# Performance work log

Hardware: AMD Instinct MI355X
Metric: run time of the kernel (lower is better)

Reference implementation:

```python
import jax, jax.numpy as jnp
import numpy as np

SMU_ALPHA = 0.25
SMU_MU = 1.0e6  # repo's act.SMU default: large mu -> smooth leaky-relu (max(x, alpha*x))

def smu(x):
    a = SMU_ALPHA
    return 0.5 * ((1.0 + a) * x + (1.0 - a) * x * jax.lax.erf(SMU_MU * (1.0 - a) * x))

def setup_inputs() -> dict:
    key = jax.random.key(0)
    ks = jax.random.split(key, 6)
    B, N, D = 8, 4096, 1024
    xavier = float(np.sqrt(6.0 / (D + D)))
    def lin_w(k):
        return jax.random.uniform(k, (D, D), jnp.float32, -xavier, xavier)
    return {
        "x": jax.random.normal(ks[0], (B, N, D), jnp.float32),
        "Wvr": lin_w(ks[1]), "bvr": jnp.zeros((D,), jnp.float32),
        "Wvi": lin_w(ks[2]), "bvi": jnp.zeros((D,), jnp.float32),
        "Wk": lin_w(ks[3]), "bk": jnp.zeros((D,), jnp.float32),
        "Wq": lin_w(ks[4]), "bq": jnp.zeros((D,), jnp.float32),
    }

def reference(x, Wvr, bvr, Wvi, bvi, Wk, bk, Wq, bq):
    # real input: real and imag branches both see x
    value_real = jnp.einsum('bnd,ed->bne', x, Wvr) + bvr
    value_imag = jnp.einsum('bnd,ed->bne', x, Wvi) + bvi
    # GLU: v_real * tanh(softplus(v_imag)); dropout disabled (p=0)
    value = value_real * jnp.tanh(jax.nn.softplus(value_imag))
    key_ = jnp.einsum('bnd,ed->bne', x, Wk) + bk
    query = jnp.einsum('bnd,ed->bne', x, Wq) + bq
    # L2 normalize along the sequence dim (dim=1)
    key_n = key_ / (jnp.linalg.norm(key_, axis=1, keepdims=True) + 1e-5)
    query_n = query / (jnp.linalg.norm(query, axis=1, keepdims=True) + 1e-5)
    feature_attn = smu(jnp.einsum('bnd,bne->bde', key_n, query_n))  # [B, D, D]
    return jnp.einsum('bnd,bde->bne', value, feature_attn)
```

## Files before the change

### kernel.cpp

```cpp
#include <hip/hip_runtime.h>
#include <math.h>

typedef __bf16 bf16x8 __attribute__((ext_vector_type(8)));
typedef float f32x4 __attribute__((ext_vector_type(4)));

#define MTOT 32768
#define DD   1024
#define NSEQ 4096
#define BB   8

__device__ __forceinline__ void async16(const void* gp, void* lp) {
  __builtin_amdgcn_global_load_lds(
      (__attribute__((address_space(1))) void*)(const_cast<void*>(gp)),
      (__attribute__((address_space(3))) void*)(lp), 16, 0, 0);
}

__device__ __forceinline__ unsigned short f2bf(float f) {
  union { float f; unsigned int u; } v; v.f = f;
  unsigned int r = v.u + 0x7fffu + ((v.u >> 16) & 1u);
  return (unsigned short)(r >> 16);
}
__device__ __forceinline__ float bf2f(unsigned short u) {
  union { unsigned int u; float f; } v; v.u = ((unsigned int)u) << 16; return v.f;
}

__device__ __forceinline__ unsigned lds_off(void* p) {
  return (unsigned)(unsigned long long)
      (__attribute__((address_space(3))) void*)p;
}
#define DSRI(dst, base, off) \
  asm volatile("ds_read_b128 %0, %1 offset:" #off : "=v"(dst) : "v"(base))

#define MFMA_ __builtin_amdgcn_mfma_f32_16x16x32_bf16

__global__ void cvt_bf16(const float* __restrict__ in, unsigned short* __restrict__ out, int n) {
  int i = (blockIdx.x * blockDim.x + threadIdx.x) * 8;
  if (i >= n) return;
  float4 a = *(const float4*)(in + i);
  float4 b = *(const float4*)(in + i + 4);
  ushort4 o0, o1;
  o0.x = f2bf(a.x); o0.y = f2bf(a.y); o0.z = f2bf(a.z); o0.w = f2bf(a.w);
  o1.x = f2bf(b.x); o1.y = f2bf(b.y); o1.z = f2bf(b.z); o1.w = f2bf(b.w);
  *(ushort4*)(out + i) = o0;
  *(ushort4*)(out + i + 4) = o1;
}

__global__ void cvt_w(const float* __restrict__ w0, const float* __restrict__ w1,
                      const float* __restrict__ w2, const float* __restrict__ w3,
                      unsigned short* __restrict__ out) {
  int z = blockIdx.y;
  const float* in = (z == 0) ? w0 : (z == 1) ? w1 : (z == 2) ? w2 : w3;
  int i = (blockIdx.x * blockDim.x + threadIdx.x) * 8;
  float4 a = *(const float4*)(in + i);
  float4 b = *(const float4*)(in + i + 4);
  ushort4 o0, o1;
  o0.x = f2bf(a.x); o0.y = f2bf(a.y); o0.z = f2bf(a.z); o0.w = f2bf(a.w);
  o1.x = f2bf(b.x); o1.y = f2bf(b.y); o1.z = f2bf(b.z); o1.w = f2bf(b.w);
  unsigned short* o = out + (size_t)z * DD * DD;
  *(ushort4*)(o + i) = o0;
  *(ushort4*)(o + i + 4) = o1;
}

template<int LDG>
__device__ __forceinline__ void stage32(const unsigned short* __restrict__ g,
                                        int row0, int k0,
                                        unsigned short* lds, int tid) {
#pragma unroll
  for (int l = 0; l < 2; ++l) {
    int u = l * 512 + tid;
    int r = u >> 2;
    int c = u & 3;
    async16(g + (size_t)(row0 + r) * LDG + k0 + c * 8, (char*)lds + u * 16);
  }
}

template<int LDG>
__device__ __forceinline__ void stage_half(const unsigned short* __restrict__ g,
                                           int row0, int k0,
                                           unsigned short* lds, int tid) {
#pragma unroll
  for (int l = 0; l < 2; ++l) {
    int u = l * 512 + tid;
    int r = u >> 3;
    int sl = (u & 7) ^ (r & 7);
    async16(g + (size_t)(row0 + r) * LDG + k0 + sl * 8, (char*)lds + u * 16);
  }
}

__global__ __launch_bounds__(512, 2) void proj_all(
    const unsigned short* __restrict__ xb,
    const unsigned short* __restrict__ Wb,
    const float* __restrict__ bvr, const float* __restrict__ bvi,
    const float* __restrict__ bk,  const float* __restrict__ bq,
    unsigned short* __restrict__ oVr, unsigned short* __restrict__ oVi,
    unsigned short* __restrict__ Kt,  unsigned short* __restrict__ Qt,
    float* __restrict__ rnacc) {
  __shared__ __align__(16) unsigned short smem[49152];

  const int bx = blockIdx.x;
  const int swz = (bx & 7) * 64 + (bx >> 3);
  const int m0 = (swz >> 2) * 256;
  const int n0 = (swz & 3) * 256;
  const int z = blockIdx.z;
  const unsigned short* W = Wb + (size_t)z * DD * DD;
  const float* bias = (z == 0) ? bvr : (z == 1) ? bvi : (z == 2) ? bk : bq;

  const int tid = threadIdx.x;
  const int w = tid >> 6, lane = tid & 63;
  const int wr = w >> 2, wc = w & 3;
  const int lq = lane >> 4, lr = lane & 15;
  const int arow0 = wr * 128 + lr;
  const int brow0 = wc * 64 + lr;

  f32x4 acc[8][4];
#pragma unroll
  for (int i = 0; i < 8; i++)
#pragma unroll
    for (int j = 0; j < 4; j++) acc[i][j] = (f32x4)(0.f);

  const int NT = 32;

  const unsigned sbase = lds_off(smem);
  unsigned aA[3], aB[3];
#pragma unroll
  for (int i = 0; i < 3; ++i) {
    aA[i] = sbase + i * 32768u + (unsigned)(arow0 * 64 + lq * 16);
    aB[i] = sbase + i * 32768u + 32768u / 2u + (unsigned)(brow0 * 64 + lq * 16);
  }

  bf16x8 A1[4], B0[2][4], A2[2][4];

  stage32<1024>(xb, m0, 0,  smem,                tid);
  stage32<1024>(W,  n0, 0,  smem + 8192,         tid);
  stage32<1024>(xb, m0, 32, smem + 16384,        tid);
  stage32<1024>(W,  n0, 32, smem + 16384 + 8192, tid);
  asm volatile("s_waitcnt vmcnt(4)" ::: "memory");
  __builtin_amdgcn_s_barrier();

  DSRI(A1[0],    aA[0], 0);    DSRI(A1[1],    aA[0], 1024);
  DSRI(A1[2],    aA[0], 2048); DSRI(A1[3],    aA[0], 3072);
  DSRI(B0[0][0], aB[0], 0);    DSRI(B0[0][1], aB[0], 1024);
  DSRI(B0[0][2], aB[0], 2048); DSRI(B0[0][3], aB[0], 3072);
  DSRI(A2[0][0], aA[0], 4096); DSRI(A2[0][1], aA[0], 5120);
  DSRI(A2[0][2], aA[0], 6144); DSRI(A2[0][3], aA[0], 7168);
  asm volatile("s_waitcnt lgkmcnt(4)" ::: "memory");
  __builtin_amdgcn_sched_barrier(0);
  __builtin_amdgcn_s_setprio(1);
#pragma unroll
  for (int mi = 0; mi < 4; ++mi)
#pragma unroll
    for (int nj = 0; nj < 4; ++nj)
      acc[mi][nj] = MFMA_(A1[mi], B0[0][nj], acc[mi][nj], 0, 0, 0);
  __builtin_amdgcn_s_setprio(0);
  __builtin_amdgcn_sched_barrier(0);
  asm volatile("s_waitcnt vmcnt(0)" ::: "memory");
  __builtin_amdgcn_s_barrier();

#pragma unroll
  for (int k = 0; k < NT - 1; ++k) {
    const int cs = k & 1, ns = (k + 1) & 1;
    const unsigned rA = aA[(k + 1) % 3], rB = aB[(k + 1) % 3];
    DSRI(A1[0],     rA, 0);    DSRI(A1[1],     rA, 1024);
    DSRI(A1[2],     rA, 2048); DSRI(A1[3],     rA, 3072);
    DSRI(B0[ns][0], rB, 0);    DSRI(B0[ns][1], rB, 1024);
    DSRI(B0[ns][2], rB, 2048); DSRI(B0[ns][3], rB, 3072);
    DSRI(A2[ns][0], rA, 4096); DSRI(A2[ns][1], rA, 5120);
    DSRI(A2[ns][2], rA, 6144); DSRI(A2[ns][3], rA, 7168);
    if (k + 2 < NT) {
      unsigned short* d = smem + ((k + 2) % 3) * 16384;
      stage32<1024>(xb, m0, (k + 2) * 32, d,        tid);
      stage32<1024>(W,  n0, (k + 2) * 32, d + 8192, tid);
    }
    asm volatile("s_waitcnt lgkmcnt(12)" ::: "memory");
    __builtin_amdgcn_sched_barrier(0);
    __builtin_amdgcn_s_setprio(1);
#pragma unroll
    for (int mi = 0; mi < 4; ++mi)
#pragma unroll
      for (int nj = 0; nj < 4; ++nj)
        acc[4 + mi][nj] = MFMA_(A2[cs][mi], B0[cs][nj], acc[4 + mi][nj], 0, 0, 0);
    __builtin_amdgcn_s_setprio(0);
    __builtin_amdgcn_sched_barrier(0);
    asm volatile("s_waitcnt lgkmcnt(4)" ::: "memory");
    __builtin_amdgcn_sched_barrier(0);
    __builtin_amdgcn_s_setprio(1);
#pragma unroll
    for (int mi = 0; mi < 4; ++mi)
#pragma unroll
      for (int nj = 0; nj < 4; ++nj)
        acc[mi][nj] = MFMA_(A1[mi], B0[ns][nj], acc[mi][nj], 0, 0, 0);
    __builtin_amdgcn_s_setprio(0);
    __builtin_amdgcn_sched_barrier(0);
    asm volatile("s_waitcnt vmcnt(0)" ::: "memory");
    __builtin_amdgcn_s_barrier();
  }
  asm volatile("s_waitcnt lgkmcnt(0)" ::: "memory");
  __builtin_amdgcn_sched_barrier(0);
#pragma unroll
  for (int mi = 0; mi < 4; ++mi)
#pragma unroll
    for (int nj = 0; nj < 4; ++nj)
      acc[4 + mi][nj] = MFMA_(A2[1][mi], B0[1][nj], acc[4 + mi][nj], 0, 0, 0);

  if (z < 2) {
    unsigned short* out = (z == 0) ? oVr : oVi;
#pragma unroll
    for (int nj = 0; nj < 4; ++nj) {
      int col = n0 + wc * 64 + nj * 16 + lr;
      float bv = bias[col];
#pragma unroll
      for (int mrep = 0; mrep < 8; ++mrep) {
        int rowb = m0 + wr * 128 + mrep * 16 + lq * 4;
#pragma unroll
        for (int r = 0; r < 4; ++r)
          out[(size_t)(rowb + r) * DD + col] = f2bf(acc[mrep][nj][r] + bv);
      }
    }
  } else {
    __syncthreads();
    unsigned short* outp = (z == 2) ? Kt : Qt;
    const int which = z - 2;
    const int b = m0 >> 12;
    const int nbase = m0 & 4095;
    float* racc = rnacc + which * (BB * DD) + b * DD;
    unsigned short* T = smem;
    const int SP2 = 264;
#pragma unroll
    for (int ch = 0; ch < 2; ++ch) {
      if ((wc >> 1) == ch) {
#pragma unroll
        for (int nj = 0; nj < 4; ++nj) {
          int cloc = (wc & 1) * 64 + nj * 16 + lr;
          float bv = bias[n0 + ch * 128 + cloc];
#pragma unroll
          for (int mrep = 0; mrep < 8; ++mrep) {
            int rowb = wr * 128 + mrep * 16 + lq * 4;
            ushort4 pk;
            pk.x = f2bf(acc[mrep][nj][0] + bv); pk.y = f2bf(acc[mrep][nj][1] + bv);
            pk.z = f2bf(acc[mrep][nj][2] + bv); pk.w = f2bf(acc[mrep][nj][3] + bv);
            *(ushort4*)(T + cloc * SP2 + rowb) = pk;
          }
        }
      }
      __syncthreads();
#pragma unroll
      for (int p = 0; p < 8; ++p) {
        int dl = p * 16 + (tid >> 5);
        int nc = (tid & 31) * 8;
        ushort4 v0 = *(const ushort4*)(T + dl * SP2 + nc);
        ushort4 v1 = *(const ushort4*)(T + dl * SP2 + nc + 4);
        int d = n0 + ch * 128 + dl;
        *(ushort4*)(outp + (size_t)(b * DD + d) * NSEQ + nbase + nc)     = v0;
        *(ushort4*)(outp + (size_t)(b * DD + d) * NSEQ + nbase + nc + 4) = v1;
        float s = bf2f(v0.x)*bf2f(v0.x) + bf2f(v0.y)*bf2f(v0.y) + bf2f(v0.z)*bf2f(v0.z) + bf2f(v0.w)*bf2f(v0.w)
                + bf2f(v1.x)*bf2f(v1.x) + bf2f(v1.y)*bf2f(v1.y) + bf2f(v1.z)*bf2f(v1.z) + bf2f(v1.w)*bf2f(v1.w);
#pragma unroll
        for (int off = 1; off < 32; off <<= 1) s += __shfl_xor(s, off, 32);
        if ((tid & 31) == 0) atomicAdd(&racc[d], s);
      }
      __syncthreads();
    }
  }
}

__global__ void finalize_rn(float* __restrict__ rn) {
  int i = blockIdx.x * blockDim.x + threadIdx.x;
  rn[i] = 1.f / (sqrtf(rn[i]) + 1e-5f);
}

__global__ void glu(unsigned short* __restrict__ V, const unsigned short* __restrict__ Vi, int n) {
  int i = (blockIdx.x * blockDim.x + threadIdx.x) * 8;
  if (i >= n) return;
  ushort4 r0 = *(const ushort4*)(V + i);
  ushort4 r1 = *(const ushort4*)(V + i + 4);
  ushort4 i0 = *(const ushort4*)(Vi + i);
  ushort4 i1 = *(const ushort4*)(Vi + i + 4);
  unsigned short vr[8] = {r0.x, r0.y, r0.z, r0.w, r1.x, r1.y, r1.z, r1.w};
  unsigned short vi[8] = {i0.x, i0.y, i0.z, i0.w, i1.x, i1.y, i1.z, i1.w};
  unsigned short o[8];
#pragma unroll
  for (int k = 0; k < 8; k++) {
    float a = bf2f(vr[k]), b = bf2f(vi[k]);
    float g;
    if (b > 10.f) g = 1.f;
    else { float t = __expf(b); float u = t * (t + 2.f); g = u / (u + 2.f); }
    o[k] = f2bf(a * g);
  }
  *(ushort4*)(V + i)     = make_ushort4(o[0], o[1], o[2], o[3]);
  *(ushort4*)(V + i + 4) = make_ushort4(o[4], o[5], o[6], o[7]);
}

__global__ __launch_bounds__(512, 2) void attn_gemm(
    const unsigned short* __restrict__ Qt, const unsigned short* __restrict__ Kt,
    const float* __restrict__ rn, unsigned short* __restrict__ fat) {
  __shared__ __align__(16) unsigned short smem[57344];

  const int b = blockIdx.z;
  const int d0 = blockIdx.x * 128;
  const int e0 = blockIdx.y * 256;
  const unsigned short* A  = Qt + (size_t)b * DD * NSEQ;
  const unsigned short* Bm = Kt + (size_t)b * DD * NSEQ;
  unsigned short* out = fat + (size_t)b * DD * DD;

  const int tid = threadIdx.x;
  const int w = tid >> 6, lane = tid & 63;
  const int wr = w >> 1, wc = w & 1;
  const int lq = lane >> 4, lr = lane & 15;
  const int sx = lr & 7;
  const int arow0 = wr * 64 + lr;
  const int brow0 = wc * 64 + lr;

  f32x4 acc[4][4];
#pragma unroll
  for (int i = 0; i < 4; i++)
#pragma unroll
    for (int j = 0; j < 4; j++) acc[i][j] = (f32x4)(0.f);

  const int NT = 64;

  const unsigned sbase = lds_off(smem);
  const unsigned sw0 = (unsigned)((lq ^ sx) << 4);
  const unsigned sw1 = (unsigned)(((4 | lq) ^ sx) << 4);
  unsigned aA0 = sbase + arow0 * 128 + sw0;
  unsigned aA1 = sbase + arow0 * 128 + sw1;
  unsigned aB0 = sbase + 32768 + brow0 * 128 + sw0;
  unsigned aB1 = sbase + 32768 + brow0 * 128 + sw1;

  stage_half<NSEQ>(A,  e0,       0,  smem,                 tid);
  stage_half<NSEQ>(A,  e0 + 128, 0,  smem + 8192,          tid);
  stage_half<NSEQ>(Bm, d0,       0,  smem + 16384,         tid);
  stage_half<NSEQ>(Bm, d0,       64, smem + 32768 + 16384, tid);
  asm volatile("s_waitcnt vmcnt(2)" ::: "memory");
  __builtin_amdgcn_s_barrier();

  for (int t = 0; t < NT; ++t) {
    bf16x8 bfr[4][2], aL[2][2];
    DSRI(aL[0][0], aA0, 0);    DSRI(aL[0][1], aA1, 0);
    DSRI(bfr[0][0], aB0, 0);    DSRI(bfr[0][1], aB1, 0);
    DSRI(bfr[1][0], aB0, 2048); DSRI(bfr[1][1], aB1, 2048);
    DSRI(bfr[2][0], aB0, 4096); DSRI(bfr[2][1], aB1, 4096);
    DSRI(bfr[3][0], aB0, 6144); DSRI(bfr[3][1], aB1, 6144);
    DSRI(aL[1][0], aA0, 2048); DSRI(aL[1][1], aA1, 2048);
    if (t + 1 < NT) {
      stage_half<NSEQ>(A, e0,       (t + 1) * 64, smem + ((t + 1) & 1) * 32768, tid);
      stage_half<NSEQ>(A, e0 + 128, (t + 1) * 64, smem + ((t + 1) & 1) * 32768 + 8192, tid);
    }
    __builtin_amdgcn_s_barrier();
    asm volatile("s_waitcnt lgkmcnt(2)" ::: "memory");
    __builtin_amdgcn_sched_barrier(0);
    __builtin_amdgcn_s_setprio(1);
#pragma unroll
    for (int nj = 0; nj < 4; ++nj) {
      acc[0][nj] = MFMA_(aL[0][0], bfr[nj][0], acc[0][nj], 0, 0, 0);
      acc[0][nj] = MFMA_(aL[0][1], bfr[nj][1], acc[0][nj], 0, 0, 0);
    }
    asm volatile("s_waitcnt lgkmcnt(0)" ::: "memory");
    __builtin_amdgcn_sched_barrier(0);
#pragma unroll
    for (int nj = 0; nj < 4; ++nj) {
      acc[1][nj] = MFMA_(aL[1][0], bfr[nj][0], acc[1][nj], 0, 0, 0);
      acc[1][nj] = MFMA_(aL[1][1], bfr[nj][1], acc[1][nj], 0, 0, 0);
    }
    __builtin_amdgcn_s_setprio(0);
    __builtin_amdgcn_sched_barrier(0);
    __builtin_amdgcn_s_barrier();

    bf16x8 aH[2][2];
    DSRI(aH[0][0], aA0, 4096); DSRI(aH[0][1], aA1, 4096);
    DSRI(aH[1][0], aA0, 6144); DSRI(aH[1][1], aA1, 6144);
    if (t + 2 < NT) {
      stage_half<NSEQ>(Bm, d0, (t + 2) * 64, smem + (t & 1) * 32768 + 16384, tid);
    }
    __builtin_amdgcn_s_barrier();
    asm volatile("s_waitcnt lgkmcnt(2)" ::: "memory");
    __builtin_amdgcn_sched_barrier(0);
    __builtin_amdgcn_s_setprio(1);
#pragma unroll
    for (int nj = 0; nj < 4; ++nj) {
      acc[2][nj] = MFMA_(aH[0][0], bfr[nj][0], acc[2][nj], 0, 0, 0);
      acc[2][nj] = MFMA_(aH[0][1], bfr[nj][1], acc[2][nj], 0, 0, 0);
    }
    asm volatile("s_waitcnt lgkmcnt(0)" ::: "memory");
    __builtin_amdgcn_sched_barrier(0);
#pragma unroll
    for (int nj = 0; nj < 4; ++nj) {
      acc[3][nj] = MFMA_(aH[1][0], bfr[nj][0], acc[3][nj], 0, 0, 0);
      acc[3][nj] = MFMA_(aH[1][1], bfr[nj][1], acc[3][nj], 0, 0, 0);
    }
    __builtin_amdgcn_s_setprio(0);
    __builtin_amdgcn_sched_barrier(0);
    if (t < NT - 2)       asm volatile("s_waitcnt vmcnt(2)" ::: "memory");
    else if (t == NT - 2) asm volatile("s_waitcnt vmcnt(0)" ::: "memory");
    __builtin_amdgcn_s_barrier();

    aA0 ^= 65536u; aA1 ^= 65536u; aB0 ^= 65536u; aB1 ^= 65536u;
  }

#pragma unroll
  for (int nj = 0; nj < 4; ++nj) {
    int col = d0 + wc * 64 + nj * 16 + lr;
    float rk = rn[b * DD + col];
#pragma unroll
    for (int mi = 0; mi < 4; ++mi) {
      int rowb = e0 + wr * 64 + mi * 16 + lq * 4;
#pragma unroll
      for (int r = 0; r < 4; ++r) {
        float rq = rn[BB * DD + b * DD + rowb + r];
        float c = acc[mi][nj][r] * rq * rk;
        c = (c > 0.f) ? c : 0.25f * c;
        out[(size_t)(rowb + r) * DD + col] = f2bf(c);
      }
    }
  }
}

__global__ __launch_bounds__(512, 2) void out_gemm(
    const unsigned short* __restrict__ V, const unsigned short* __restrict__ fat,
    float* __restrict__ out) {
  __shared__ __align__(16) unsigned short smem[49152];

  const int bx = blockIdx.x;
  const int swz = (bx & 7) * 64 + (bx >> 3);
  const int m0 = (swz >> 2) * 256;
  const int e0 = (swz & 3) * 256;
  const int b = m0 >> 12;
  const unsigned short* Bm = fat + (size_t)b * DD * DD;

  const int tid = threadIdx.x;
  const int w = tid >> 6, lane = tid & 63;
  const int wr = w >> 2, wc = w & 3;
  const int lq = lane >> 4, lr = lane & 15;
  const int arow0 = wr * 128 + lr;
  const int brow0 = wc * 64 + lr;

  f32x4 acc[8][4];
#pragma unroll
  for (int i = 0; i < 8; i++)
#pragma unroll
    for (int j = 0; j < 4; j++) acc[i][j] = (f32x4)(0.f);

  const int NT = 32;

  const unsigned sbase = lds_off(smem);
  unsigned aA[3], aB[3];
#pragma unroll
  for (int i = 0; i < 3; ++i) {
    aA[i] = sbase + i * 32768u + (unsigned)(arow0 * 64 + lq * 16);
    aB[i] = sbase + i * 32768u + 16384u + (unsigned)(brow0 * 64 + lq * 16);
  }

  bf16x8 A1[4], B0[2][4], A2[2][4];

  stage32<1024>(V,  m0, 0,  smem,                tid);
  stage32<1024>(Bm, e0, 0,  smem + 8192,         tid);
  stage32<1024>(V,  m0, 32, smem + 16384,        tid);
  stage32<1024>(Bm, e0, 32, smem + 16384 + 8192, tid);
  asm volatile("s_waitcnt vmcnt(4)" ::: "memory");
  __builtin_amdgcn_s_barrier();

  DSRI(A1[0],    aA[0], 0);    DSRI(A1[1],    aA[0], 1024);
  DSRI(A1[2],    aA[0], 2048); DSRI(A1[3],    aA[0], 3072);
  DSRI(B0[0][0], aB[0], 0);    DSRI(B0[0][1], aB[0], 1024);
  DSRI(B0[0][2], aB[0], 2048); DSRI(B0[0][3], aB[0], 3072);
  DSRI(A2[0][0], aA[0], 4096); DSRI(A2[0][1], aA[0], 5120);
  DSRI(A2[0][2], aA[0], 6144); DSRI(A2[0][3], aA[0], 7168);
  asm volatile("s_waitcnt lgkmcnt(4)" ::: "memory");
  __builtin_amdgcn_sched_barrier(0);
  __builtin_amdgcn_s_setprio(1);
#pragma unroll
  for (int mi = 0; mi < 4; ++mi)
#pragma unroll
    for (int nj = 0; nj < 4; ++nj)
      acc[mi][nj] = MFMA_(A1[mi], B0[0][nj], acc[mi][nj], 0, 0, 0);
  __builtin_amdgcn_s_setprio(0);
  __builtin_amdgcn_sched_barrier(0);
  asm volatile("s_waitcnt vmcnt(0)" ::: "memory");
  __builtin_amdgcn_s_barrier();

#pragma unroll
  for (int k = 0; k < NT - 1; ++k) {
    const int cs = k & 1, ns = (k + 1) & 1;
    const unsigned rA = aA[(k + 1) % 3], rB = aB[(k + 1) % 3];
    DSRI(A1[0],     rA, 0);    DSRI(A1[1],     rA, 1024);
    DSRI(A1[2],     rA, 2048); DSRI(A1[3],     rA, 3072);
    DSRI(B0[ns][0], rB, 0);    DSRI(B0[ns][1], rB, 1024);
    DSRI(B0[ns][2], rB, 2048); DSRI(B0[ns][3], rB, 3072);
    DSRI(A2[ns][0], rA, 4096); DSRI(A2[ns][1], rA, 5120);
    DSRI(A2[ns][2], rA, 6144); DSRI(A2[ns][3], rA, 7168);
    if (k + 2 < NT) {
      unsigned short* d = smem + ((k + 2) % 3) * 16384;
      stage32<1024>(V,  m0, (k + 2) * 32, d,        tid);
      stage32<1024>(Bm, e0, (k + 2) * 32, d + 8192, tid);
    }
    asm volatile("s_waitcnt lgkmcnt(12)" ::: "memory");
    __builtin_amdgcn_sched_barrier(0);
    __builtin_amdgcn_s_setprio(1);
#pragma unroll
    for (int mi = 0; mi < 4; ++mi)
#pragma unroll
      for (int nj = 0; nj < 4; ++nj)
        acc[4 + mi][nj] = MFMA_(A2[cs][mi], B0[cs][nj], acc[4 + mi][nj], 0, 0, 0);
    __builtin_amdgcn_s_setprio(0);
    __builtin_amdgcn_sched_barrier(0);
    asm volatile("s_waitcnt lgkmcnt(4)" ::: "memory");
    __builtin_amdgcn_sched_barrier(0);
    __builtin_amdgcn_s_setprio(1);
#pragma unroll
    for (int mi = 0; mi < 4; ++mi)
#pragma unroll
      for (int nj = 0; nj < 4; ++nj)
        acc[mi][nj] = MFMA_(A1[mi], B0[ns][nj], acc[mi][nj], 0, 0, 0);
    __builtin_amdgcn_s_setprio(0);
    __builtin_amdgcn_sched_barrier(0);
    asm volatile("s_waitcnt vmcnt(0)" ::: "memory");
    __builtin_amdgcn_s_barrier();
  }
  asm volatile("s_waitcnt lgkmcnt(0)" ::: "memory");
  __builtin_amdgcn_sched_barrier(0);
#pragma unroll
  for (int mi = 0; mi < 4; ++mi)
#pragma unroll
    for (int nj = 0; nj < 4; ++nj)
      acc[4 + mi][nj] = MFMA_(A2[1][mi], B0[1][nj], acc[4 + mi][nj], 0, 0, 0);

#pragma unroll
  for (int nj = 0; nj < 4; ++nj) {
    int col = e0 + wc * 64 + nj * 16 + lr;
#pragma unroll
    for (int mrep = 0; mrep < 8; ++mrep) {
      int rowb = m0 + wr * 128 + mrep * 16 + lq * 4;
#pragma unroll
      for (int r = 0; r < 4; ++r)
        out[(size_t)(rowb + r) * DD + col] = acc[mrep][nj][r];
    }
  }
}

extern "C" void kernel_launch(void* const* d_in, const int* in_sizes, int n_in,
                              void* d_out, int out_size, void* d_ws, size_t ws_size,
                              hipStream_t stream) {
  const float* x   = (const float*)d_in[0];
  const float* Wvr = (const float*)d_in[1];
  const float* bvr = (const float*)d_in[2];
  const float* Wvi = (const float*)d_in[3];
  const float* bvi = (const float*)d_in[4];
  const float* Wk  = (const float*)d_in[5];
  const float* bk  = (const float*)d_in[6];
  const float* Wq  = (const float*)d_in[7];
  const float* bq  = (const float*)d_in[8];
  float* out = (float*)d_out;

  char* p = (char*)d_ws;
  unsigned short* xb  = (unsigned short*)p; p += (size_t)MTOT * DD * 2;
  unsigned short* Wb  = (unsigned short*)p; p += 4ull * DD * DD * 2;
  unsigned short* Kt  = (unsigned short*)p; p += (size_t)BB * DD * NSEQ * 2;
  unsigned short* Qt  = (unsigned short*)p; p += (size_t)BB * DD * NSEQ * 2;
  unsigned short* Vb  = (unsigned short*)p; p += (size_t)MTOT * DD * 2;
  unsigned short* fat = (unsigned short*)p; p += (size_t)BB * DD * DD * 2;
  float* rn = (float*)p; p += 2ull * BB * DD * sizeof(float);

  unsigned short* ViBuf = (unsigned short*)d_out;

  int nx = MTOT * DD;
  int nw = DD * DD;
  cvt_bf16<<<nx / 8 / 256, 256, 0, stream>>>(x, xb, nx);
  cvt_w<<<dim3(nw / 8 / 256, 4), 256, 0, stream>>>(Wvr, Wvi, Wk, Wq, Wb);
  hipMemsetAsync(rn, 0, 2ull * BB * DD * sizeof(float), stream);

  proj_all<<<dim3(512, 1, 4), 512, 0, stream>>>(
      xb, Wb, bvr, bvi, bk, bq, Vb, ViBuf, Kt, Qt, rn);

  glu<<<nx / 8 / 256, 256, 0, stream>>>(Vb, ViBuf, nx);
  finalize_rn<<<2 * BB * DD / 256, 256, 0, stream>>>(rn);

  attn_gemm<<<dim3(DD / 128, DD / 256, BB), 512, 0, stream>>>(Qt, Kt, rn, fat);
  out_gemm<<<dim3(512), 512, 0, stream>>>(Vb, fat, out);
}
```

Baseline: 761.2 us.

## Shrink proj and out GEMM tiles to 128x128 with 4 waves and swizzled LDS

```diff
diff --git a/kernel.cpp b/kernel.cpp
--- a/kernel.cpp
+++ b/kernel.cpp
@@ -62,15 +62,16 @@
 }
 
 template<int LDG>
-__device__ __forceinline__ void stage32(const unsigned short* __restrict__ g,
-                                        int row0, int k0,
-                                        unsigned short* lds, int tid) {
+__device__ __forceinline__ void stage128(const unsigned short* __restrict__ g,
+                                         int row0, int k0,
+                                         unsigned short* lds, int tid) {
 #pragma unroll
   for (int l = 0; l < 2; ++l) {
-    int u = l * 512 + tid;
+    int u = l * 256 + tid;
     int r = u >> 2;
     int c = u & 3;
-    async16(g + (size_t)(row0 + r) * LDG + k0 + c * 8, (char*)lds + u * 16);
+    int sl = c ^ ((r >> 1) & 3);
+    async16(g + (size_t)(row0 + r) * LDG + k0 + sl * 8, (char*)lds + u * 16);
   }
 }
 
@@ -87,7 +88,7 @@
   }
 }
 
-__global__ __launch_bounds__(512, 2) void proj_all(
+__global__ __launch_bounds__(256, 4) void proj_all(
     const unsigned short* __restrict__ xb,
     const unsigned short* __restrict__ Wb,
     const float* __restrict__ bvr, const float* __restrict__ bvi,
@@ -95,112 +96,83 @@
     unsigned short* __restrict__ oVr, unsigned short* __restrict__ oVi,
     unsigned short* __restrict__ Kt,  unsigned short* __restrict__ Qt,
     float* __restrict__ rnacc) {
-  __shared__ __align__(16) unsigned short smem[49152];
+  __shared__ __align__(16) unsigned short smem[18432];
 
   const int bx = blockIdx.x;
-  const int swz = (bx & 7) * 64 + (bx >> 3);
-  const int m0 = (swz >> 2) * 256;
-  const int n0 = (swz & 3) * 256;
+  const int swz = (bx & 7) * 256 + (bx >> 3);
+  const int m0 = (swz >> 3) * 128;
+  const int n0 = (swz & 7) * 128;
   const int z = blockIdx.z;
   const unsigned short* W = Wb + (size_t)z * DD * DD;
   const float* bias = (z == 0) ? bvr : (z == 1) ? bvi : (z == 2) ? bk : bq;
 
   const int tid = threadIdx.x;
   const int w = tid >> 6, lane = tid & 63;
-  const int wr = w >> 2, wc = w & 3;
+  const int wr = w >> 1, wc = w & 1;
   const int lq = lane >> 4, lr = lane & 15;
-  const int arow0 = wr * 128 + lr;
+  const int key = (lr >> 1) & 3;
+  const int arow0 = wr * 64 + lr;
   const int brow0 = wc * 64 + lr;
 
-  f32x4 acc[8][4];
-#pragma unroll
-  for (int i = 0; i < 8; i++)
+  f32x4 acc[4][4];
+#pragma unroll
+  for (int i = 0; i < 4; i++)
 #pragma unroll
     for (int j = 0; j < 4; j++) acc[i][j] = (f32x4)(0.f);
 
   const int NT = 32;
 
   const unsigned sbase = lds_off(smem);
-  unsigned aA[3], aB[3];
-#pragma unroll
-  for (int i = 0; i < 3; ++i) {
-    aA[i] = sbase + i * 32768u + (unsigned)(arow0 * 64 + lq * 16);
-    aB[i] = sbase + i * 32768u + 32768u / 2u + (unsigned)(brow0 * 64 + lq * 16);
-  }
-
-  bf16x8 A1[4], B0[2][4], A2[2][4];
-
-  stage32<1024>(xb, m0, 0,  smem,                tid);
-  stage32<1024>(W,  n0, 0,  smem + 8192,         tid);
-  stage32<1024>(xb, m0, 32, smem + 16384,        tid);
-  stage32<1024>(W,  n0, 32, smem + 16384 + 8192, tid);
+  const unsigned swsl = (unsigned)((lq ^ key) << 4);
+  unsigned aA[2], aB[2];
+#pragma unroll
+  for (int i = 0; i < 2; ++i) {
+    aA[i] = sbase + i * 16384u + (unsigned)(arow0 * 64) + swsl;
+    aB[i] = sbase + i * 16384u + 8192u + (unsigned)(brow0 * 64) + swsl;
+  }
+
+  stage128<1024>(xb, m0, 0,  smem,               tid);
+  stage128<1024>(W,  n0, 0,  smem + 4096,        tid);
+  stage128<1024>(xb, m0, 32, smem + 8192,        tid);
+  stage128<1024>(W,  n0, 32, smem + 8192 + 4096, tid);
   asm volatile("s_waitcnt vmcnt(4)" ::: "memory");
   __builtin_amdgcn_s_barrier();
 
-  DSRI(A1[0],    aA[0], 0);    DSRI(A1[1],    aA[0], 1024);
-  DSRI(A1[2],    aA[0], 2048); DSRI(A1[3],    aA[0], 3072);
-  DSRI(B0[0][0], aB[0], 0);    DSRI(B0[0][1], aB[0], 1024);
-  DSRI(B0[0][2], aB[0], 2048); DSRI(B0[0][3], aB[0], 3072);
-  DSRI(A2[0][0], aA[0], 4096); DSRI(A2[0][1], aA[0], 5120);
-  DSRI(A2[0][2], aA[0], 6144); DSRI(A2[0][3], aA[0], 7168);
-  asm volatile("s_waitcnt lgkmcnt(4)" ::: "memory");
-  __builtin_amdgcn_sched_barrier(0);
-  __builtin_amdgcn_s_setprio(1);
-#pragma unroll
-  for (int mi = 0; mi < 4; ++mi)
+#pragma unroll
+  for (int k = 0; k < NT; ++k) {
+    const unsigned rA = aA[k & 1], rB = aB[k & 1];
+    bf16x8 Af[4], Bf[4];
+    DSRI(Af[0], rA, 0);
+    DSRI(Bf[0], rB, 0);    DSRI(Bf[1], rB, 1024);
+    DSRI(Bf[2], rB, 2048); DSRI(Bf[3], rB, 3072);
+    DSRI(Af[1], rA, 1024); DSRI(Af[2], rA, 2048); DSRI(Af[3], rA, 3072);
+    asm volatile("s_waitcnt lgkmcnt(3)" ::: "memory");
+    __builtin_amdgcn_sched_barrier(0);
+    __builtin_amdgcn_s_setprio(1);
 #pragma unroll
     for (int nj = 0; nj < 4; ++nj)
-      acc[mi][nj] = MFMA_(A1[mi], B0[0][nj], acc[mi][nj], 0, 0, 0);
-  __builtin_amdgcn_s_setprio(0);
-  __builtin_amdgcn_sched_barrier(0);
-  asm volatile("s_waitcnt vmcnt(0)" ::: "memory");
-  __builtin_amdgcn_s_barrier();
-
-#pragma unroll
-  for (int k = 0; k < NT - 1; ++k) {
-    const int cs = k & 1, ns = (k + 1) & 1;
-    const unsigned rA = aA[(k + 1) % 3], rB = aB[(k + 1) % 3];
-    DSRI(A1[0],     rA, 0);    DSRI(A1[1],     rA, 1024);
-    DSRI(A1[2],     rA, 2048); DSRI(A1[3],     rA, 3072);
-    DSRI(B0[ns][0], rB, 0);    DSRI(B0[ns][1], rB, 1024);
-    DSRI(B0[ns][2], rB, 2048); DSRI(B0[ns][3], rB, 3072);
-    DSRI(A2[ns][0], rA, 4096); DSRI(A2[ns][1], rA, 5120);
-    DSRI(A2[ns][2], rA, 6144); DSRI(A2[ns][3], rA, 7168);
+      acc[0][nj] = MFMA_(Af[0], Bf[nj], acc[0][nj], 0, 0, 0);
+    asm volatile("s_waitcnt lgkmcnt(0)" ::: "memory");
+    __builtin_amdgcn_sched_barrier(0);
+#pragma unroll
+    for (int mi = 1; mi < 4; ++mi)
+#pragma unroll
+      for (int nj = 0; nj < 4; ++nj)
+        acc[mi][nj] = MFMA_(Af[mi], Bf[nj], acc[mi][nj], 0, 0, 0);
+    __builtin_amdgcn_s_setprio(0);
+    __builtin_amdgcn_sched_barrier(0);
+    __builtin_amdgcn_s_barrier();
     if (k + 2 < NT) {
-      unsigned short* d = smem + ((k + 2) % 3) * 16384;
-      stage32<1024>(xb, m0, (k + 2) * 32, d,        tid);
-      stage32<1024>(W,  n0, (k + 2) * 32, d + 8192, tid);
-    }
-    asm volatile("s_waitcnt lgkmcnt(12)" ::: "memory");
-    __builtin_amdgcn_sched_barrier(0);
-    __builtin_amdgcn_s_setprio(1);
-#pragma unroll
-    for (int mi = 0; mi < 4; ++mi)
-#pragma unroll
-      for (int nj = 0; nj < 4; ++nj)
-        acc[4 + mi][nj] = MFMA_(A2[cs][mi], B0[cs][nj], acc[4 + mi][nj], 0, 0, 0);
-    __builtin_amdgcn_s_setprio(0);
-    __builtin_amdgcn_sched_barrier(0);
-    asm volatile("s_waitcnt lgkmcnt(4)" ::: "memory");
-    __builtin_amdgcn_sched_barrier(0);
-    __builtin_amdgcn_s_setprio(1);
-#pragma unroll
-    for (int mi = 0; mi < 4; ++mi)
-#pragma unroll
-      for (int nj = 0; nj < 4; ++nj)
-        acc[mi][nj] = MFMA_(A1[mi], B0[ns][nj], acc[mi][nj], 0, 0, 0);
-    __builtin_amdgcn_s_setprio(0);
-    __builtin_amdgcn_sched_barrier(0);
-    asm volatile("s_waitcnt vmcnt(0)" ::: "memory");
-    __builtin_amdgcn_s_barrier();
-  }
-  asm volatile("s_waitcnt lgkmcnt(0)" ::: "memory");
-  __builtin_amdgcn_sched_barrier(0);
-#pragma unroll
-  for (int mi = 0; mi < 4; ++mi)
-#pragma unroll
-    for (int nj = 0; nj < 4; ++nj)
-      acc[4 + mi][nj] = MFMA_(A2[1][mi], B0[1][nj], acc[4 + mi][nj], 0, 0, 0);
+      unsigned short* d = smem + (k & 1) * 8192;
+      stage128<1024>(xb, m0, (k + 2) * 32, d,        tid);
+      stage128<1024>(W,  n0, (k + 2) * 32, d + 4096, tid);
+    }
+    if (k + 1 < NT) {
+      if (k + 2 < NT) asm volatile("s_waitcnt vmcnt(4)" ::: "memory");
+      else            asm volatile("s_waitcnt vmcnt(0)" ::: "memory");
+      __builtin_amdgcn_s_barrier();
+    }
+  }
 
   if (z < 2) {
     unsigned short* out = (z == 0) ? oVr : oVi;
@@ -209,11 +181,11 @@
       int col = n0 + wc * 64 + nj * 16 + lr;
       float bv = bias[col];
 #pragma unroll
-      for (int mrep = 0; mrep < 8; ++mrep) {
-        int rowb = m0 + wr * 128 + mrep * 16 + lq * 4;
+      for (int mi = 0; mi < 4; ++mi) {
+        int rowb = m0 + wr * 64 + mi * 16 + lq * 4;
 #pragma unroll
         for (int r = 0; r < 4; ++r)
-          out[(size_t)(rowb + r) * DD + col] = f2bf(acc[mrep][nj][r] + bv);
+          out[(size_t)(rowb + r) * DD + col] = f2bf(acc[mi][nj][r] + bv);
       }
     }
   } else {
@@ -224,41 +196,35 @@
     const int nbase = m0 & 4095;
     float* racc = rnacc + which * (BB * DD) + b * DD;
     unsigned short* T = smem;
-    const int SP2 = 264;
-#pragma unroll
-    for (int ch = 0; ch < 2; ++ch) {
-      if ((wc >> 1) == ch) {
-#pragma unroll
-        for (int nj = 0; nj < 4; ++nj) {
-          int cloc = (wc & 1) * 64 + nj * 16 + lr;
-          float bv = bias[n0 + ch * 128 + cloc];
-#pragma unroll
-          for (int mrep = 0; mrep < 8; ++mrep) {
-            int rowb = wr * 128 + mrep * 16 + lq * 4;
-            ushort4 pk;
-            pk.x = f2bf(acc[mrep][nj][0] + bv); pk.y = f2bf(acc[mrep][nj][1] + bv);
-            pk.z = f2bf(acc[mrep][nj][2] + bv); pk.w = f2bf(acc[mrep][nj][3] + bv);
-            *(ushort4*)(T + cloc * SP2 + rowb) = pk;
-          }
-        }
+    const int SP2 = 136;
+#pragma unroll
+    for (int nj = 0; nj < 4; ++nj) {
+      int cloc = wc * 64 + nj * 16 + lr;
+      float bv = bias[n0 + cloc];
+#pragma unroll
+      for (int mi = 0; mi < 4; ++mi) {
+        int rowb = wr * 64 + mi * 16 + lq * 4;
+        ushort4 pk;
+        pk.x = f2bf(acc[mi][nj][0] + bv); pk.y = f2bf(acc[mi][nj][1] + bv);
+        pk.z = f2bf(acc[mi][nj][2] + bv); pk.w = f2bf(acc[mi][nj][3] + bv);
+        *(ushort4*)(T + cloc * SP2 + rowb) = pk;
       }
-      __syncthreads();
-#pragma unroll
-      for (int p = 0; p < 8; ++p) {
-        int dl = p * 16 + (tid >> 5);
-        int nc = (tid & 31) * 8;
-        ushort4 v0 = *(const ushort4*)(T + dl * SP2 + nc);
-        ushort4 v1 = *(const ushort4*)(T + dl * SP2 + nc + 4);
-        int d = n0 + ch * 128 + dl;
-        *(ushort4*)(outp + (size_t)(b * DD + d) * NSEQ + nbase + nc)     = v0;
-        *(ushort4*)(outp + (size_t)(b * DD + d) * NSEQ + nbase + nc + 4) = v1;
-        float s = bf2f(v0.x)*bf2f(v0.x) + bf2f(v0.y)*bf2f(v0.y) + bf2f(v0.z)*bf2f(v0.z) + bf2f(v0.w)*bf2f(v0.w)
-                + bf2f(v1.x)*bf2f(v1.x) + bf2f(v1.y)*bf2f(v1.y) + bf2f(v1.z)*bf2f(v1.z) + bf2f(v1.w)*bf2f(v1.w);
-#pragma unroll
-        for (int off = 1; off < 32; off <<= 1) s += __shfl_xor(s, off, 32);
-        if ((tid & 31) == 0) atomicAdd(&racc[d], s);
-      }
-      __syncthreads();
+    }
+    __syncthreads();
+#pragma unroll
+    for (int p = 0; p < 8; ++p) {
+      int dl = p * 16 + (tid >> 4);
+      int nc = (tid & 15) * 8;
+      ushort4 v0 = *(const ushort4*)(T + dl * SP2 + nc);
+      ushort4 v1 = *(const ushort4*)(T + dl * SP2 + nc + 4);
+      int d = n0 + dl;
+      *(ushort4*)(outp + (size_t)(b * DD + d) * NSEQ + nbase + nc)     = v0;
+      *(ushort4*)(outp + (size_t)(b * DD + d) * NSEQ + nbase + nc + 4) = v1;
+      float s = bf2f(v0.x)*bf2f(v0.x) + bf2f(v0.y)*bf2f(v0.y) + bf2f(v0.z)*bf2f(v0.z) + bf2f(v0.w)*bf2f(v0.w)
+              + bf2f(v1.x)*bf2f(v1.x) + bf2f(v1.y)*bf2f(v1.y) + bf2f(v1.z)*bf2f(v1.z) + bf2f(v1.w)*bf2f(v1.w);
+#pragma unroll
+      for (int off = 1; off < 16; off <<= 1) s += __shfl_xor(s, off, 16);
+      if ((tid & 15) == 0) atomicAdd(&racc[d], s);
     }
   }
 }
@@ -414,124 +380,95 @@
   }
 }
 
-__global__ __launch_bounds__(512, 2) void out_gemm(
+__global__ __launch_bounds__(256, 4) void out_gemm(
     const unsigned short* __restrict__ V, const unsigned short* __restrict__ fat,
     float* __restrict__ out) {
-  __shared__ __align__(16) unsigned short smem[49152];
+  __shared__ __align__(16) unsigned short smem[18432];
 
   const int bx = blockIdx.x;
-  const int swz = (bx & 7) * 64 + (bx >> 3);
-  const int m0 = (swz >> 2) * 256;
-  const int e0 = (swz & 3) * 256;
+  const int swz = (bx & 7) * 256 + (bx >> 3);
+  const int m0 = (swz >> 3) * 128;
+  const int e0 = (swz & 7) * 128;
   const int b = m0 >> 12;
   const unsigned short* Bm = fat + (size_t)b * DD * DD;
 
   const int tid = threadIdx.x;
   const int w = tid >> 6, lane = tid & 63;
-  const int wr = w >> 2, wc = w & 3;
+  const int wr = w >> 1, wc = w & 1;
   const int lq = lane >> 4, lr = lane & 15;
-  const int arow0 = wr * 128 + lr;
+  const int key = (lr >> 1) & 3;
+  const int arow0 = wr * 64 + lr;
   const int brow0 = wc * 64 + lr;
 
-  f32x4 acc[8][4];
-#pragma unroll
-  for (int i = 0; i < 8; i++)
+  f32x4 acc[4][4];
+#pragma unroll
+  for (int i = 0; i < 4; i++)
 #pragma unroll
     for (int j = 0; j < 4; j++) acc[i][j] = (f32x4)(0.f);
 
   const int NT = 32;
 
   const unsigned sbase = lds_off(smem);
-  unsigned aA[3], aB[3];
-#pragma unroll
-  for (int i = 0; i < 3; ++i) {
-    aA[i] = sbase + i * 32768u + (unsigned)(arow0 * 64 + lq * 16);
-    aB[i] = sbase + i * 32768u + 16384u + (unsigned)(brow0 * 64 + lq * 16);
-  }
-
-  bf16x8 A1[4], B0[2][4], A2[2][4];
-
-  stage32<1024>(V,  m0, 0,  smem,                tid);
-  stage32<1024>(Bm, e0, 0,  smem + 8192,         tid);
-  stage32<1024>(V,  m0, 32, smem + 16384,        tid);
-  stage32<1024>(Bm, e0, 32, smem + 16384 + 8192, tid);
+  const unsigned swsl = (unsigned)((lq ^ key) << 4);
+  unsigned aA[2], aB[2];
+#pragma unroll
+  for (int i = 0; i < 2; ++i) {
+    aA[i] = sbase + i * 16384u + (unsigned)(arow0 * 64) + swsl;
+    aB[i] = sbase + i * 16384u + 8192u + (unsigned)(brow0 * 64) + swsl;
+  }
+
+  stage128<1024>(V,  m0, 0,  smem,               tid);
+  stage128<1024>(Bm, e0, 0,  smem + 4096,        tid);
+  stage128<1024>(V,  m0, 32, smem + 8192,        tid);
+  stage128<1024>(Bm, e0, 32, smem + 8192 + 4096, tid);
   asm volatile("s_waitcnt vmcnt(4)" ::: "memory");
   __builtin_amdgcn_s_barrier();
 
-  DSRI(A1[0],    aA[0], 0);    DSRI(A1[1],    aA[0], 1024);
-  DSRI(A1[2],    aA[0], 2048); DSRI(A1[3],    aA[0], 3072);
-  DSRI(B0[0][0], aB[0], 0);    DSRI(B0[0][1], aB[0], 1024);
-  DSRI(B0[0][2], aB[0], 2048); DSRI(B0[0][3], aB[0], 3072);
-  DSRI(A2[0][0], aA[0], 4096); DSRI(A2[0][1], aA[0], 5120);
-  DSRI(A2[0][2], aA[0], 6144); DSRI(A2[0][3], aA[0], 7168);
-  asm volatile("s_waitcnt lgkmcnt(4)" ::: "memory");
-  __builtin_amdgcn_sched_barrier(0);
-  __builtin_amdgcn_s_setprio(1);
-#pragma unroll
-  for (int mi = 0; mi < 4; ++mi)
+#pragma unroll
+  for (int k = 0; k < NT; ++k) {
+    const unsigned rA = aA[k & 1], rB = aB[k & 1];
+    bf16x8 Af[4], Bf[4];
+    DSRI(Af[0], rA, 0);
+    DSRI(Bf[0], rB, 0);    DSRI(Bf[1], rB, 1024);
+    DSRI(Bf[2], rB, 2048); DSRI(Bf[3], rB, 3072);
+    DSRI(Af[1], rA, 1024); DSRI(Af[2], rA, 2048); DSRI(Af[3], rA, 3072);
+    asm volatile("s_waitcnt lgkmcnt(3)" ::: "memory");
+    __builtin_amdgcn_sched_barrier(0);
+    __builtin_amdgcn_s_setprio(1);
 #pragma unroll
     for (int nj = 0; nj < 4; ++nj)
-      acc[mi][nj] = MFMA_(A1[mi], B0[0][nj], acc[mi][nj], 0, 0, 0);
-  __builtin_amdgcn_s_setprio(0);
-  __builtin_amdgcn_sched_barrier(0);
-  asm volatile("s_waitcnt vmcnt(0)" ::: "memory");
-  __builtin_amdgcn_s_barrier();
-
-#pragma unroll
-  for (int k = 0; k < NT - 1; ++k) {
-    const int cs = k & 1, ns = (k + 1) & 1;
-    const unsigned rA = aA[(k + 1) % 3], rB = aB[(k + 1) % 3];
-    DSRI(A1[0],     rA, 0);    DSRI(A1[1],     rA, 1024);
-    DSRI(A1[2],     rA, 2048); DSRI(A1[3],     rA, 3072);
-    DSRI(B0[ns][0], rB, 0);    DSRI(B0[ns][1], rB, 1024);
-    DSRI(B0[ns][2], rB, 2048); DSRI(B0[ns][3], rB, 3072);
-    DSRI(A2[ns][0], rA, 4096); DSRI(A2[ns][1], rA, 5120);
-    DSRI(A2[ns][2], rA, 6144); DSRI(A2[ns][3], rA, 7168);
+      acc[0][nj] = MFMA_(Af[0], Bf[nj], acc[0][nj], 0, 0, 0);
+    asm volatile("s_waitcnt lgkmcnt(0)" ::: "memory");
+    __builtin_amdgcn_sched_barrier(0);
+#pragma unroll
+    for (int mi = 1; mi < 4; ++mi)
+#pragma unroll
+      for (int nj = 0; nj < 4; ++nj)
+        acc[mi][nj] = MFMA_(Af[mi], Bf[nj], acc[mi][nj], 0, 0, 0);
+    __builtin_amdgcn_s_setprio(0);
+    __builtin_amdgcn_sched_barrier(0);
+    __builtin_amdgcn_s_barrier();
     if (k + 2 < NT) {
-      unsigned short* d = smem + ((k + 2) % 3) * 16384;
-      stage32<1024>(V,  m0, (k + 2) * 32, d,        tid);
-      stage32<1024>(Bm, e0, (k + 2) * 32, d + 8192, tid);
-    }
-    asm volatile("s_waitcnt lgkmcnt(12)" ::: "memory");
-    __builtin_amdgcn_sched_barrier(0);
-    __builtin_amdgcn_s_setprio(1);
-#pragma unroll
-    for (int mi = 0; mi < 4; ++mi)
-#pragma unroll
-      for (int nj = 0; nj < 4; ++nj)
-        acc[4 + mi][nj] = MFMA_(A2[cs][mi], B0[cs][nj], acc[4 + mi][nj], 0, 0, 0);
-    __builtin_amdgcn_s_setprio(0);
-    __builtin_amdgcn_sched_barrier(0);
-    asm volatile("s_waitcnt lgkmcnt(4)" ::: "memory");
-    __builtin_amdgcn_sched_barrier(0);
-    __builtin_amdgcn_s_setprio(1);
-#pragma unroll
-    for (int mi = 0; mi < 4; ++mi)
-#pragma unroll
-      for (int nj = 0; nj < 4; ++nj)
-        acc[mi][nj] = MFMA_(A1[mi], B0[ns][nj], acc[mi][nj], 0, 0, 0);
-    __builtin_amdgcn_s_setprio(0);
-    __builtin_amdgcn_sched_barrier(0);
-    asm volatile("s_waitcnt vmcnt(0)" ::: "memory");
-    __builtin_amdgcn_s_barrier();
-  }
-  asm volatile("s_waitcnt lgkmcnt(0)" ::: "memory");
-  __builtin_amdgcn_sched_barrier(0);
-#pragma unroll
-  for (int mi = 0; mi < 4; ++mi)
-#pragma unroll
-    for (int nj = 0; nj < 4; ++nj)
-      acc[4 + mi][nj] = MFMA_(A2[1][mi], B0[1][nj], acc[4 + mi][nj], 0, 0, 0);
+      unsigned short* d = smem + (k & 1) * 8192;
+      stage128<1024>(V,  m0, (k + 2) * 32, d,        tid);
+      stage128<1024>(Bm, e0, (k + 2) * 32, d + 4096, tid);
+    }
+    if (k + 1 < NT) {
+      if (k + 2 < NT) asm volatile("s_waitcnt vmcnt(4)" ::: "memory");
+      else            asm volatile("s_waitcnt vmcnt(0)" ::: "memory");
+      __builtin_amdgcn_s_barrier();
+    }
+  }
 
 #pragma unroll
   for (int nj = 0; nj < 4; ++nj) {
     int col = e0 + wc * 64 + nj * 16 + lr;
 #pragma unroll
-    for (int mrep = 0; mrep < 8; ++mrep) {
-      int rowb = m0 + wr * 128 + mrep * 16 + lq * 4;
+    for (int mi = 0; mi < 4; ++mi) {
+      int rowb = m0 + wr * 64 + mi * 16 + lq * 4;
 #pragma unroll
       for (int r = 0; r < 4; ++r)
-        out[(size_t)(rowb + r) * DD + col] = acc[mrep][nj][r];
+        out[(size_t)(rowb + r) * DD + col] = acc[mi][nj][r];
     }
   }
 }
@@ -567,12 +504,12 @@
   cvt_w<<<dim3(nw / 8 / 256, 4), 256, 0, stream>>>(Wvr, Wvi, Wk, Wq, Wb);
   hipMemsetAsync(rn, 0, 2ull * BB * DD * sizeof(float), stream);
 
-  proj_all<<<dim3(512, 1, 4), 512, 0, stream>>>(
+  proj_all<<<dim3(2048, 1, 4), 256, 0, stream>>>(
       xb, Wb, bvr, bvi, bk, bq, Vb, ViBuf, Kt, Qt, rn);
 
   glu<<<nx / 8 / 256, 256, 0, stream>>>(Vb, ViBuf, nx);
   finalize_rn<<<2 * BB * DD / 256, 256, 0, stream>>>(rn);
 
   attn_gemm<<<dim3(DD / 128, DD / 256, BB), 512, 0, stream>>>(Qt, Kt, rn, fat);
-  out_gemm<<<dim3(512), 512, 0, stream>>>(Vb, fat, out);
-}
+  out_gemm<<<dim3(2048), 256, 0, stream>>>(Vb, fat, out);
+}
```

New measurement: 767.9 us. Within noise of the previous version (+0.9%).
